# Optimization experiments

Hardware: AMD Instinct MI355X
Metric: run time of the kernel (lower is better)

## Reference

```python
import jax, jax.numpy as jnp
import numpy as np

REG = 0.05  # reg_param > 0 -> entropic (logsumexp) branch
N, M, D = 16384, 8192, 128


def setup_inputs() -> dict:
    key = jax.random.key(0)
    k1, k2, k3 = jax.random.split(key, 3)
    source_data = jax.random.normal(k1, (N, D), dtype=jnp.float32)
    target_data = jax.random.normal(k2, (M, D), dtype=jnp.float32)
    psi = jax.random.normal(k3, (M,), dtype=jnp.float32) * 0.1
    return {"source_data": source_data, "target_data": target_data, "psi": psi}


def reference(source_data, target_data, psi):
    # squared norms
    ty2 = jnp.sum(target_data ** 2, axis=1)            # [M]
    sx2 = jnp.sum(source_data ** 2, axis=1, keepdims=True)  # [N,1]
    scale = jnp.mean(ty2)                              # scalar normalizer
    # pairwise squared-distance cost, normalized (matches torch expansion)
    cost_xy = (sx2 + ty2[None, :] - 2.0 * source_data @ target_data.T) / scale  # [N,M]
    # entropic semi-dual: -reg * logsumexp((psi - c)/reg) averaged over x
    lse = jax.nn.logsumexp((psi[None, :] - cost_xy) / REG, axis=1)  # [N]
    cte = REG * jnp.log(jnp.asarray(M, dtype=jnp.float32))
    return jnp.mean(-REG * lse) + jnp.mean(psi) + cte
```

## Files before the change

### kernel.cpp

```cpp
#include <hip/hip_runtime.h>
#include <stdint.h>

#define REG_P   0.05f
#define LOG2E   1.4426950408889634f
#define LN2     0.6931471805599453f
#define NSPLIT  8

typedef int   int32x8 __attribute__((ext_vector_type(8)));
typedef float floatx4 __attribute__((ext_vector_type(4)));

__device__ inline int32x8 load32B(const void* p) {
    union { int32x8 v; uint4 q[2]; } u;
    u.q[0] = ((const uint4*)p)[0];
    u.q[1] = ((const uint4*)p)[1];
    return u.v;
}

__device__ inline float sum32(const float* __restrict__ p, int lane) {
    float v = p[lane & 31];
    #pragma unroll
    for (int mask = 1; mask < 32; mask <<= 1) v += __shfl_xor(v, mask, 64);
    return v;
}

__global__ void k1_pack(const float* __restrict__ src, const float* __restrict__ tgt,
                        unsigned char* __restrict__ Sb8, unsigned char* __restrict__ Tbs8,
                        float* __restrict__ sx2, float* __restrict__ ty2,
                        int N, int M) {
    int tid = threadIdx.x;
    int r16 = tid >> 4;
    int c8  = tid & 15;
    int row_id = blockIdx.x * 16 + r16;
    bool isS = row_id < N;
    int row = isS ? row_id : row_id - N;
    const float4* sp = (const float4*)((isS ? src : tgt) + (size_t)row * 128 + c8 * 8);
    float4 f0 = sp[0], f1 = sp[1];
    int w0 = 0, w1 = 0;
    w0 = __builtin_amdgcn_cvt_pk_fp8_f32(f0.x, f0.y, w0, false);
    w0 = __builtin_amdgcn_cvt_pk_fp8_f32(f0.z, f0.w, w0, true);
    w1 = __builtin_amdgcn_cvt_pk_fp8_f32(f1.x, f1.y, w1, false);
    w1 = __builtin_amdgcn_cvt_pk_fp8_f32(f1.z, f1.w, w1, true);
    uint2 val = make_uint2((unsigned)w0, (unsigned)w1);
    float sq = f0.x*f0.x + f0.y*f0.y + f0.z*f0.z + f0.w*f0.w
             + f1.x*f1.x + f1.y*f1.y + f1.z*f1.z + f1.w*f1.w;
    #pragma unroll
    for (int mask = 1; mask < 16; mask <<= 1) sq += __shfl_xor(sq, mask, 16);
    if (isS) {
        ((uint2*)(Sb8 + (size_t)row * 128 + c8 * 8))[0] = val;
        if (c8 == 0) sx2[row] = sq;
    } else {
        int t = row >> 6, jc = row & 63;
        int ct = jc >> 4, l16 = jc & 15;
        int quad = c8 >> 2, rem = c8 & 3;
        size_t dst = (size_t)t * 8192 + (size_t)((ct * 64 + quad * 16 + l16) * 32 + rem * 8);
        ((uint2*)(Tbs8 + dst))[0] = val;
        if (c8 == 0) ty2[row] = sq;
    }
}

__global__ void k1b_sums(const float* __restrict__ sx2, const float* __restrict__ ty2,
                         const float* __restrict__ psi, float* __restrict__ scalpart,
                         float* __restrict__ out, int N, int M) {
    __shared__ float red[3][4];
    int tid = threadIdx.x;
    int gid = blockIdx.x * 256 + tid;
    float s_sx = 0.f, s_ty = 0.f, s_ps = 0.f;
    for (int i = gid; i < N; i += 32 * 256) s_sx += sx2[i];
    for (int j = gid; j < M; j += 32 * 256) { s_ty += ty2[j]; s_ps += psi[j]; }
    #pragma unroll
    for (int off = 32; off > 0; off >>= 1) {
        s_sx += __shfl_xor(s_sx, off, 64);
        s_ty += __shfl_xor(s_ty, off, 64);
        s_ps += __shfl_xor(s_ps, off, 64);
    }
    int wv = tid >> 6, lane = tid & 63;
    if (lane == 0) { red[0][wv] = s_ty; red[1][wv] = s_sx; red[2][wv] = s_ps; }
    __syncthreads();
    if (tid == 0) {
        scalpart[blockIdx.x]      = red[0][0] + red[0][1] + red[0][2] + red[0][3];
        scalpart[32 + blockIdx.x] = red[1][0] + red[1][1] + red[1][2] + red[1][3];
        scalpart[64 + blockIdx.x] = red[2][0] + red[2][1] + red[2][2] + red[2][3];
        if (blockIdx.x == 0) out[0] = 0.0f;
    }
}

__global__ __launch_bounds__(256) void k3_main(
    const unsigned char* __restrict__ Sb8, const unsigned char* __restrict__ Tbs8,
    const float* __restrict__ psi, const float* __restrict__ ty2,
    const float* __restrict__ scalpart, float* __restrict__ lpart, int N, int M) {
    __shared__ float sb2a[1024];
    const int tid  = threadIdx.x;
    const int lane = tid & 63;
    const int wv   = tid >> 6;
    const int quad = lane >> 4, l16 = lane & 15;
    const int b = blockIdx.x;
    const int split = b & 7;
    const int i0 = (b >> 3) * 128;
    const int mspan = M / NSPLIT;
    const int jstart = split * mspan;

    float ty2sum = sum32(scalpart, lane);
    float scale = ty2sum / (float)M;
    float c1 = 1.0f / (REG_P * scale);
    float a2 = 2.0f * LOG2E / (REG_P * scale);

    for (int idx = tid; idx < mspan; idx += 256) {
        int j = jstart + idx;
        sb2a[idx] = (psi[j] * (1.0f / REG_P) - ty2[j] * c1) * LOG2E;
    }
    __syncthreads();

    int32x8 afrag[2];
    #pragma unroll
    for (int rt = 0; rt < 2; ++rt)
        afrag[rt] = load32B(Sb8 + (size_t)(i0 + wv * 32 + rt * 16 + l16) * 128 + quad * 32);

    float ls[2][4];
    #pragma unroll
    for (int rt = 0; rt < 2; ++rt)
        #pragma unroll
        for (int r = 0; r < 4; ++r) ls[rt][r] = 0.0f;

    const unsigned char* gb = Tbs8 + (size_t)jstart * 128 + (size_t)lane * 32;
    const floatx4 zero4 = (floatx4){0.f, 0.f, 0.f, 0.f};
    const int SC = 0x7F7F7F7F;

    int32x8 bbuf[2][4];
    #pragma unroll
    for (int c = 0; c < 4; ++c) bbuf[0][c] = load32B(gb + c * 2048);

    floatx4 accP0, accP1;
    float bvP = 0.0f;
    bool first = true;

    #pragma unroll 2
    for (int tt = 0; tt < 16; ++tt) {
        const int p = tt & 1;
        if (tt < 15) {
            #pragma unroll
            for (int c = 0; c < 4; ++c)
                bbuf[p ^ 1][c] = load32B(gb + (size_t)((tt + 1) * 4 + c) * 2048);
        }
        #pragma unroll
        for (int c = 0; c < 4; ++c) {
            float bv = sb2a[(tt * 4 + c) * 16 + l16];
            floatx4 a0 = __builtin_amdgcn_mfma_scale_f32_16x16x128_f8f6f4(
                afrag[0], bbuf[p][c], zero4, 0, 0, 0, SC, 0, SC);
            floatx4 a1 = __builtin_amdgcn_mfma_scale_f32_16x16x128_f8f6f4(
                afrag[1], bbuf[p][c], zero4, 0, 0, 0, SC, 0, SC);
            if (!first) {
                #pragma unroll
                for (int r = 0; r < 4; ++r) {
                    ls[0][r] += __builtin_amdgcn_exp2f(fmaf(a2, accP0[r], bvP));
                    ls[1][r] += __builtin_amdgcn_exp2f(fmaf(a2, accP1[r], bvP));
                }
            }
            accP0 = a0; accP1 = a1; bvP = bv;
            first = false;
        }
    }
    #pragma unroll
    for (int r = 0; r < 4; ++r) {
        ls[0][r] += __builtin_amdgcn_exp2f(fmaf(a2, accP0[r], bvP));
        ls[1][r] += __builtin_amdgcn_exp2f(fmaf(a2, accP1[r], bvP));
    }

    #pragma unroll
    for (int rt = 0; rt < 2; ++rt)
        #pragma unroll
        for (int r = 0; r < 4; ++r) {
            float v = ls[rt][r];
            #pragma unroll
            for (int mask = 1; mask < 16; mask <<= 1) v += __shfl_xor(v, mask, 64);
            if (l16 == 0) {
                int rowg = i0 + wv * 32 + rt * 16 + quad * 4 + r;
                lpart[(size_t)rowg * NSPLIT + split] = v;
            }
        }
}

__global__ void k4_reduce(const float* __restrict__ lpart,
                          const float* __restrict__ scalpart,
                          float* __restrict__ out, int N, int M) {
    __shared__ float red[4];
    int i = blockIdx.x * 256 + threadIdx.x;
    const float4* lp = (const float4*)(lpart + (size_t)i * NSPLIT);
    float4 p0 = lp[0], p1 = lp[1];
    float s = (p0.x + p0.y + p0.z + p0.w) + (p1.x + p1.y + p1.z + p1.w);
    float L2 = __builtin_amdgcn_logf(s);
    #pragma unroll
    for (int off = 32; off > 0; off >>= 1) L2 += __shfl_xor(L2, off, 64);
    int wv = threadIdx.x >> 6, lane = threadIdx.x & 63;
    if (lane == 0) red[wv] = L2;
    __syncthreads();
    if (threadIdx.x == 0) {
        float blocksum = red[0] + red[1] + red[2] + red[3];
        atomicAdd(out, -REG_P * LN2 / (float)N * blocksum);
    }
    if (blockIdx.x == 0) {
        float ty2s = sum32(scalpart, lane);
        float sx2s = sum32(scalpart + 32, lane);
        float psis = sum32(scalpart + 64, lane);
        if (threadIdx.x == 0) {
            float scale = ty2s / (float)M;
            atomicAdd(out, (sx2s / (float)N) / scale
                         + psis / (float)M
                         + REG_P * logf((float)M));
        }
    }
}

extern "C" void kernel_launch(void* const* d_in, const int* in_sizes, int n_in,
                              void* d_out, int out_size, void* d_ws, size_t ws_size,
                              hipStream_t stream) {
    const float* src = (const float*)d_in[0];
    const float* tgt = (const float*)d_in[1];
    const float* psi = (const float*)d_in[2];
    const int D = 128;
    const int N = in_sizes[0] / D;
    const int M = in_sizes[1] / D;

    char* ws = (char*)d_ws;
    float* scalpart = (float*)ws;
    float* sx2   = (float*)(ws + 512);
    float* ty2   = (float*)(ws + 512 + (size_t)N * 4);
    float* lpart = (float*)(ws + 512 + (size_t)N * 4 + (size_t)M * 4);
    size_t off = 512 + (size_t)N * 4 + (size_t)M * 4 + (size_t)N * NSPLIT * 4;
    off = (off + 255) & ~(size_t)255;
    unsigned char* Sb8  = (unsigned char*)(ws + off);
    unsigned char* Tbs8 = Sb8 + (size_t)N * 128;

    k1_pack<<<(N + M) / 16, 256, 0, stream>>>(src, tgt, Sb8, Tbs8, sx2, ty2, N, M);
    k1b_sums<<<32, 256, 0, stream>>>(sx2, ty2, psi, scalpart, (float*)d_out, N, M);
    k3_main<<<(N / 128) * NSPLIT, 256, 0, stream>>>(Sb8, Tbs8, psi, ty2, scalpart, lpart, N, M);
    k4_reduce<<<N / 256, 256, 0, stream>>>(lpart, scalpart, (float*)d_out, N, M);
}
```

Baseline: 104.0 us.

## Drop scalar-sum kernel, recompute ty2 sum per block, and double rows per k3 block

Removes the k1b_sums launch. Each k3 and k4 block now sums ty2 (M floats) itself, and k4 folds the sx2 and psi means into its per-row reduction. k3_main now covers 256 rows per block with 4 A fragments per wave, halving the grid and the number of times each B tile is reloaded, with launch_bounds raised to 2. The cost is redundant ty2 reduction work in every block, higher register pressure, and fewer blocks to fill the CUs.

```diff
diff --git a/kernel.cpp b/kernel.cpp
--- a/kernel.cpp
+++ b/kernel.cpp
@@ -16,18 +16,28 @@
     return u.v;
 }
 
-__device__ inline float sum32(const float* __restrict__ p, int lane) {
-    float v = p[lane & 31];
-    #pragma unroll
-    for (int mask = 1; mask < 32; mask <<= 1) v += __shfl_xor(v, mask, 64);
-    return v;
+__device__ inline float block_sum_f(const float* __restrict__ v, int M, int tid,
+                                    float* redbuf) {
+    float s = 0.f;
+    const float4* v4 = (const float4*)v;
+    for (int j = tid; j < (M >> 2); j += 256) {
+        float4 q = v4[j];
+        s += (q.x + q.y) + (q.z + q.w);
+    }
+    #pragma unroll
+    for (int mask = 1; mask < 64; mask <<= 1) s += __shfl_xor(s, mask, 64);
+    int wv = tid >> 6, lane = tid & 63;
+    if (lane == 0) redbuf[wv] = s;
+    __syncthreads();
+    return (redbuf[0] + redbuf[1]) + (redbuf[2] + redbuf[3]);
 }
 
 __global__ void k1_pack(const float* __restrict__ src, const float* __restrict__ tgt,
                         unsigned char* __restrict__ Sb8, unsigned char* __restrict__ Tbs8,
                         float* __restrict__ sx2, float* __restrict__ ty2,
-                        int N, int M) {
+                        float* __restrict__ out, int N, int M) {
     int tid = threadIdx.x;
+    if (blockIdx.x == 0 && tid == 0) out[0] = 0.0f;
     int r16 = tid >> 4;
     int c8  = tid & 15;
     int row_id = blockIdx.x * 16 + r16;
@@ -58,48 +68,23 @@
     }
 }
 
-__global__ void k1b_sums(const float* __restrict__ sx2, const float* __restrict__ ty2,
-                         const float* __restrict__ psi, float* __restrict__ scalpart,
-                         float* __restrict__ out, int N, int M) {
-    __shared__ float red[3][4];
-    int tid = threadIdx.x;
-    int gid = blockIdx.x * 256 + tid;
-    float s_sx = 0.f, s_ty = 0.f, s_ps = 0.f;
-    for (int i = gid; i < N; i += 32 * 256) s_sx += sx2[i];
-    for (int j = gid; j < M; j += 32 * 256) { s_ty += ty2[j]; s_ps += psi[j]; }
-    #pragma unroll
-    for (int off = 32; off > 0; off >>= 1) {
-        s_sx += __shfl_xor(s_sx, off, 64);
-        s_ty += __shfl_xor(s_ty, off, 64);
-        s_ps += __shfl_xor(s_ps, off, 64);
-    }
-    int wv = tid >> 6, lane = tid & 63;
-    if (lane == 0) { red[0][wv] = s_ty; red[1][wv] = s_sx; red[2][wv] = s_ps; }
-    __syncthreads();
-    if (tid == 0) {
-        scalpart[blockIdx.x]      = red[0][0] + red[0][1] + red[0][2] + red[0][3];
-        scalpart[32 + blockIdx.x] = red[1][0] + red[1][1] + red[1][2] + red[1][3];
-        scalpart[64 + blockIdx.x] = red[2][0] + red[2][1] + red[2][2] + red[2][3];
-        if (blockIdx.x == 0) out[0] = 0.0f;
-    }
-}
-
-__global__ __launch_bounds__(256) void k3_main(
+__global__ __launch_bounds__(256, 2) void k3_main(
     const unsigned char* __restrict__ Sb8, const unsigned char* __restrict__ Tbs8,
     const float* __restrict__ psi, const float* __restrict__ ty2,
-    const float* __restrict__ scalpart, float* __restrict__ lpart, int N, int M) {
+    float* __restrict__ lpart, int N, int M) {
     __shared__ float sb2a[1024];
+    __shared__ float redA[4];
     const int tid  = threadIdx.x;
     const int lane = tid & 63;
     const int wv   = tid >> 6;
     const int quad = lane >> 4, l16 = lane & 15;
     const int b = blockIdx.x;
     const int split = b & 7;
-    const int i0 = (b >> 3) * 128;
+    const int i0 = (b >> 3) * 256;
     const int mspan = M / NSPLIT;
     const int jstart = split * mspan;
 
-    float ty2sum = sum32(scalpart, lane);
+    float ty2sum = block_sum_f(ty2, M, tid, redA);
     float scale = ty2sum / (float)M;
     float c1 = 1.0f / (REG_P * scale);
     float a2 = 2.0f * LOG2E / (REG_P * scale);
@@ -110,14 +95,14 @@
     }
     __syncthreads();
 
-    int32x8 afrag[2];
-    #pragma unroll
-    for (int rt = 0; rt < 2; ++rt)
-        afrag[rt] = load32B(Sb8 + (size_t)(i0 + wv * 32 + rt * 16 + l16) * 128 + quad * 32);
-
-    float ls[2][4];
-    #pragma unroll
-    for (int rt = 0; rt < 2; ++rt)
+    int32x8 afrag[4];
+    #pragma unroll
+    for (int rt = 0; rt < 4; ++rt)
+        afrag[rt] = load32B(Sb8 + (size_t)(i0 + wv * 64 + rt * 16 + l16) * 128 + quad * 32);
+
+    float ls[4][4];
+    #pragma unroll
+    for (int rt = 0; rt < 4; ++rt)
         #pragma unroll
         for (int r = 0; r < 4; ++r) ls[rt][r] = 0.0f;
 
@@ -129,7 +114,7 @@
     #pragma unroll
     for (int c = 0; c < 4; ++c) bbuf[0][c] = load32B(gb + c * 2048);
 
-    floatx4 accP0, accP1;
+    floatx4 accP[4];
     float bvP = 0.0f;
     bool first = true;
 
@@ -144,69 +129,71 @@
         #pragma unroll
         for (int c = 0; c < 4; ++c) {
             float bv = sb2a[(tt * 4 + c) * 16 + l16];
-            floatx4 a0 = __builtin_amdgcn_mfma_scale_f32_16x16x128_f8f6f4(
-                afrag[0], bbuf[p][c], zero4, 0, 0, 0, SC, 0, SC);
-            floatx4 a1 = __builtin_amdgcn_mfma_scale_f32_16x16x128_f8f6f4(
-                afrag[1], bbuf[p][c], zero4, 0, 0, 0, SC, 0, SC);
+            floatx4 a[4];
+            #pragma unroll
+            for (int rt = 0; rt < 4; ++rt)
+                a[rt] = __builtin_amdgcn_mfma_scale_f32_16x16x128_f8f6f4(
+                    afrag[rt], bbuf[p][c], zero4, 0, 0, 0, SC, 0, SC);
             if (!first) {
                 #pragma unroll
-                for (int r = 0; r < 4; ++r) {
-                    ls[0][r] += __builtin_amdgcn_exp2f(fmaf(a2, accP0[r], bvP));
-                    ls[1][r] += __builtin_amdgcn_exp2f(fmaf(a2, accP1[r], bvP));
-                }
+                for (int rt = 0; rt < 4; ++rt)
+                    #pragma unroll
+                    for (int r = 0; r < 4; ++r)
+                        ls[rt][r] += __builtin_amdgcn_exp2f(fmaf(a2, accP[rt][r], bvP));
             }
-            accP0 = a0; accP1 = a1; bvP = bv;
+            #pragma unroll
+            for (int rt = 0; rt < 4; ++rt) accP[rt] = a[rt];
+            bvP = bv;
             first = false;
         }
     }
     #pragma unroll
-    for (int r = 0; r < 4; ++r) {
-        ls[0][r] += __builtin_amdgcn_exp2f(fmaf(a2, accP0[r], bvP));
-        ls[1][r] += __builtin_amdgcn_exp2f(fmaf(a2, accP1[r], bvP));
-    }
-
-    #pragma unroll
-    for (int rt = 0; rt < 2; ++rt)
+    for (int rt = 0; rt < 4; ++rt)
+        #pragma unroll
+        for (int r = 0; r < 4; ++r)
+            ls[rt][r] += __builtin_amdgcn_exp2f(fmaf(a2, accP[rt][r], bvP));
+
+    #pragma unroll
+    for (int rt = 0; rt < 4; ++rt)
         #pragma unroll
         for (int r = 0; r < 4; ++r) {
             float v = ls[rt][r];
             #pragma unroll
             for (int mask = 1; mask < 16; mask <<= 1) v += __shfl_xor(v, mask, 64);
             if (l16 == 0) {
-                int rowg = i0 + wv * 32 + rt * 16 + quad * 4 + r;
+                int rowg = i0 + wv * 64 + rt * 16 + quad * 4 + r;
                 lpart[(size_t)rowg * NSPLIT + split] = v;
             }
         }
 }
 
 __global__ void k4_reduce(const float* __restrict__ lpart,
-                          const float* __restrict__ scalpart,
+                          const float* __restrict__ sx2,
+                          const float* __restrict__ psi,
+                          const float* __restrict__ ty2,
                           float* __restrict__ out, int N, int M) {
-    __shared__ float red[4];
-    int i = blockIdx.x * 256 + threadIdx.x;
+    __shared__ float redA[4];
+    __shared__ float redB[4];
+    int tid = threadIdx.x;
+    float ty2s = block_sum_f(ty2, M, tid, redA);
+    float scale = ty2s / (float)M;
+
+    int i = blockIdx.x * 256 + tid;
     const float4* lp = (const float4*)(lpart + (size_t)i * NSPLIT);
     float4 p0 = lp[0], p1 = lp[1];
     float s = (p0.x + p0.y + p0.z + p0.w) + (p1.x + p1.y + p1.z + p1.w);
     float L2 = __builtin_amdgcn_logf(s);
-    #pragma unroll
-    for (int off = 32; off > 0; off >>= 1) L2 += __shfl_xor(L2, off, 64);
-    int wv = threadIdx.x >> 6, lane = threadIdx.x & 63;
-    if (lane == 0) red[wv] = L2;
+    float t = (-REG_P * LN2 * L2 + sx2[i] / scale) * (1.0f / (float)N);
+    if (i < M) t += psi[i] * (1.0f / (float)M);
+    #pragma unroll
+    for (int mask = 1; mask < 64; mask <<= 1) t += __shfl_xor(t, mask, 64);
+    int wv = tid >> 6, lane = tid & 63;
+    if (lane == 0) redB[wv] = t;
     __syncthreads();
-    if (threadIdx.x == 0) {
-        float blocksum = red[0] + red[1] + red[2] + red[3];
-        atomicAdd(out, -REG_P * LN2 / (float)N * blocksum);
-    }
-    if (blockIdx.x == 0) {
-        float ty2s = sum32(scalpart, lane);
-        float sx2s = sum32(scalpart + 32, lane);
-        float psis = sum32(scalpart + 64, lane);
-        if (threadIdx.x == 0) {
-            float scale = ty2s / (float)M;
-            atomicAdd(out, (sx2s / (float)N) / scale
-                         + psis / (float)M
-                         + REG_P * logf((float)M));
-        }
+    if (tid == 0) {
+        float total = (redB[0] + redB[1]) + (redB[2] + redB[3]);
+        if (blockIdx.x == 0) total += REG_P * logf((float)M);
+        atomicAdd(out, total);
     }
 }
 
@@ -221,17 +208,16 @@
     const int M = in_sizes[1] / D;
 
     char* ws = (char*)d_ws;
-    float* scalpart = (float*)ws;
-    float* sx2   = (float*)(ws + 512);
-    float* ty2   = (float*)(ws + 512 + (size_t)N * 4);
-    float* lpart = (float*)(ws + 512 + (size_t)N * 4 + (size_t)M * 4);
-    size_t off = 512 + (size_t)N * 4 + (size_t)M * 4 + (size_t)N * NSPLIT * 4;
+    float* sx2   = (float*)ws;
+    float* ty2   = (float*)(ws + (size_t)N * 4);
+    float* lpart = (float*)(ws + (size_t)N * 4 + (size_t)M * 4);
+    size_t off = (size_t)N * 4 + (size_t)M * 4 + (size_t)N * NSPLIT * 4;
     off = (off + 255) & ~(size_t)255;
     unsigned char* Sb8  = (unsigned char*)(ws + off);
     unsigned char* Tbs8 = Sb8 + (size_t)N * 128;
 
-    k1_pack<<<(N + M) / 16, 256, 0, stream>>>(src, tgt, Sb8, Tbs8, sx2, ty2, N, M);
-    k1b_sums<<<32, 256, 0, stream>>>(sx2, ty2, psi, scalpart, (float*)d_out, N, M);
-    k3_main<<<(N / 128) * NSPLIT, 256, 0, stream>>>(Sb8, Tbs8, psi, ty2, scalpart, lpart, N, M);
-    k4_reduce<<<N / 256, 256, 0, stream>>>(lpart, scalpart, (float*)d_out, N, M);
-}
+    k1_pack<<<(N + M) / 16, 256, 0, stream>>>(src, tgt, Sb8, Tbs8, sx2, ty2,
+                                              (float*)d_out, N, M);
+    k3_main<<<(N / 256) * NSPLIT, 256, 0, stream>>>(Sb8, Tbs8, psi, ty2, lpart, N, M);
+    k4_reduce<<<N / 256, 256, 0, stream>>>(lpart, sx2, psi, ty2, (float*)d_out, N, M);
+}
```

After: 100.2 us. 3.7% less time.
